# Kernel tuning notes

Measured on AMD Instinct MI355X. Metric: run time of the kernel, lower is better.

Reference implementation:

```python
import jax, jax.numpy as jnp
import numpy as np

N_HEAD = 16


def setup_inputs() -> dict:
    key = jax.random.key(0)
    ks = jax.random.split(key, 11)
    B, T, D = 8, 448, 1024
    init = 0.02
    x = jax.random.normal(ks[0], (B, T, D), dtype=jnp.float32)
    k_cache = jax.random.normal(ks[1], (B, T, D), dtype=jnp.float32)
    v_cache = jax.random.normal(ks[2], (B, T, D), dtype=jnp.float32)
    # Whisper-style additive causal mask: 0 on/below diagonal, large negative above
    mask = jnp.triu(jnp.full((T, T), -1e9, dtype=jnp.float32), k=1)
    Wq = jax.random.normal(ks[3], (D, D), dtype=jnp.float32) * init
    bq = jax.random.normal(ks[4], (D,), dtype=jnp.float32) * init
    Wk = jax.random.normal(ks[5], (D, D), dtype=jnp.float32) * init  # key proj has no bias
    Wv = jax.random.normal(ks[6], (D, D), dtype=jnp.float32) * init
    bv = jax.random.normal(ks[7], (D,), dtype=jnp.float32) * init
    Wo = jax.random.normal(ks[8], (D, D), dtype=jnp.float32) * init
    bo = jax.random.normal(ks[9], (D,), dtype=jnp.float32) * init
    return {"x": x, "k_cache": k_cache, "v_cache": v_cache, "mask": mask,
            "Wq": Wq, "bq": bq, "Wk": Wk, "Wv": Wv, "bv": bv, "Wo": Wo, "bo": bo}


def reference(x, k_cache, v_cache, mask, Wq, bq, Wk, Wv, bv, Wo, bo):
    # QKV projections (key has no bias, as in Whisper)
    q = x @ Wq + bq
    k = x @ Wk
    v = x @ Wv + bv
    # In-place KV cache append: write new keys/values into the tail of the cache
    T_new = k.shape[1]
    k_cache = k_cache.at[:, -T_new:, :].set(k)
    v_cache = v_cache.at[:, -T_new:, :].set(v)

    B, T, D = q.shape
    H = N_HEAD
    dh = D // H
    scale = dh ** (-0.25)  # applied to BOTH q and k

    qh = (q * scale).reshape(B, T, H, dh).transpose(0, 2, 1, 3)           # [B,H,T,dh]
    kh = (k_cache * scale).reshape(B, k_cache.shape[1], H, dh).transpose(0, 2, 1, 3)
    vh = v_cache.reshape(B, v_cache.shape[1], H, dh).transpose(0, 2, 1, 3)

    qk = jnp.einsum('bhqd,bhkd->bhqk', qh, kh) + mask[:T, :T]             # [B,H,T,Tc]
    qk = qk.astype(jnp.float32)  # upcast for softmax, matching original
    w = jax.nn.softmax(qk, axis=-1).astype(q.dtype)

    out = jnp.einsum('bhqk,bhkd->bhqd', w, vh)                            # [B,H,T,dh]
    out = out.transpose(0, 2, 1, 3).reshape(B, T, D)
    return out @ Wo + bo, k_cache, v_cache
```

## Files before the change

### kernel.cpp

```cpp
#include <hip/hip_runtime.h>
#include <hip/hip_bf16.h>
#include <math.h>

#define B 8
#define T 448
#define D 1024
#define H 16
#define DH 64
#define M (B*T)

typedef short short8 __attribute__((ext_vector_type(8)));
typedef float floatx4 __attribute__((ext_vector_type(4)));
typedef unsigned short u16;

__device__ __forceinline__ u16 f2bf(float f) {
    union { float f; unsigned u; } v; v.f = f;
    unsigned r = v.u + 0x7FFF + ((v.u >> 16) & 1);
    return (u16)(r >> 16);
}

__global__ __launch_bounds__(256) void xconv(const float* __restrict__ x, u16* __restrict__ xb) {
    const int i = blockIdx.x * 256 + threadIdx.x;
    float4 v = ((const float4*)x)[i];
    ushort4 o;
    o.x = f2bf(v.x); o.y = f2bf(v.y); o.z = f2bf(v.z); o.w = f2bf(v.w);
    ((ushort4*)xb)[i] = o;
}

__global__ __launch_bounds__(256) void wconv(const float* __restrict__ W, u16* __restrict__ Wt) {
    __shared__ float tile[64][65];
    const int k0 = blockIdx.y * 64, n0 = blockIdx.x * 64;
    const int tr = threadIdx.x >> 4;
    const int tc = threadIdx.x & 15;
    #pragma unroll
    for (int i = 0; i < 4; ++i) {
        float4 v = *(const float4*)(W + (size_t)(k0 + tr + 16 * i) * D + n0 + tc * 4);
        tile[tr + 16 * i][tc * 4 + 0] = v.x;
        tile[tr + 16 * i][tc * 4 + 1] = v.y;
        tile[tr + 16 * i][tc * 4 + 2] = v.z;
        tile[tr + 16 * i][tc * 4 + 3] = v.w;
    }
    __syncthreads();
    #pragma unroll
    for (int i = 0; i < 4; ++i) {
        const int n = tr + 16 * i;
        ushort4 o;
        o.x = f2bf(tile[tc * 4 + 0][n]);
        o.y = f2bf(tile[tc * 4 + 1][n]);
        o.z = f2bf(tile[tc * 4 + 2][n]);
        o.w = f2bf(tile[tc * 4 + 3][n]);
        *(ushort4*)(Wt + (size_t)(n0 + n) * D + k0 + tc * 4) = o;
    }
}

#define GBM 128
#define GBN 64
#define GBK 32
__global__ __launch_bounds__(256) void gemm_bt(
    const u16* __restrict__ A, const u16* __restrict__ Bt,
    const float* __restrict__ bias,
    float* __restrict__ Cf,
    u16* __restrict__ Cb)
{
    __shared__ u16 As[GBM][GBK + 8];
    __shared__ u16 Bs[GBN][GBK + 8];
    const int m0 = blockIdx.y * GBM;
    const int n0 = blockIdx.x * GBN;
    const int tid = threadIdx.x;
    const int wave = tid >> 6, lane = tid & 63;
    const int wy = wave >> 1, wx = wave & 1;
    const int lrow = lane & 15, lquad = lane >> 4;

    floatx4 acc[4][2];
    #pragma unroll
    for (int i = 0; i < 4; ++i)
        #pragma unroll
        for (int j = 0; j < 2; ++j)
            acc[i][j] = (floatx4){0.f, 0.f, 0.f, 0.f};

    const int sa = tid * 2;
    for (int k0 = 0; k0 < 1024; k0 += GBK) {
        short8 a0 = *(const short8*)(A + (size_t)(m0 + (sa >> 2)) * 1024 + k0 + (sa & 3) * 8);
        short8 a1 = *(const short8*)(A + (size_t)(m0 + ((sa + 1) >> 2)) * 1024 + k0 + ((sa + 1) & 3) * 8);
        short8 b0 = *(const short8*)(Bt + (size_t)(n0 + (tid >> 2)) * 1024 + k0 + (tid & 3) * 8);
        __syncthreads();
        *(short8*)&As[sa >> 2][(sa & 3) * 8] = a0;
        *(short8*)&As[(sa + 1) >> 2][((sa + 1) & 3) * 8] = a1;
        *(short8*)&Bs[tid >> 2][(tid & 3) * 8] = b0;
        __syncthreads();
        short8 af[4], bfr[2];
        #pragma unroll
        for (int i = 0; i < 4; ++i)
            af[i] = *(const short8*)&As[wy * 64 + i * 16 + lrow][lquad * 8];
        #pragma unroll
        for (int j = 0; j < 2; ++j)
            bfr[j] = *(const short8*)&Bs[wx * 32 + j * 16 + lrow][lquad * 8];
        #pragma unroll
        for (int i = 0; i < 4; ++i)
            #pragma unroll
            for (int j = 0; j < 2; ++j)
                acc[i][j] = __builtin_amdgcn_mfma_f32_16x16x32_bf16(af[i], bfr[j], acc[i][j], 0, 0, 0);
    }

    #pragma unroll
    for (int j = 0; j < 2; ++j) {
        const int col = n0 + wx * 32 + j * 16 + lrow;
        const float bb = bias ? bias[col] : 0.f;
        #pragma unroll
        for (int i = 0; i < 4; ++i) {
            #pragma unroll
            for (int r = 0; r < 4; ++r) {
                const int row = m0 + wy * 64 + i * 16 + lquad * 4 + r;
                const float v = acc[i][j][r] + bb;
                if (Cf) Cf[(size_t)row * 1024 + col] = v;
                if (Cb) Cb[(size_t)row * 1024 + col] = f2bf(v);
            }
        }
    }
}

__global__ __launch_bounds__(256) void flash_attn(
    const u16* __restrict__ Qb, const u16* __restrict__ Kb,
    const u16* __restrict__ Vb, u16* __restrict__ Ob)
{
    __shared__ u16 Qs[64][72];
    __shared__ u16 Ks[64][72];
    __shared__ u16 Vt[64][72];
    __shared__ u16 Pt[4][16][72];
    const int qt = blockIdx.x;
    const int bh = blockIdx.y;
    const int h = bh & (H - 1), b = bh >> 4;
    const int tid = threadIdx.x, wave = tid >> 6, lane = tid & 63;
    const int lrow = lane & 15, lquad = lane >> 4;
    const int q0 = qt * 64;

    const size_t hoff = (size_t)h * DH;
    const u16* qbase = Qb + (size_t)b * T * D + hoff;
    const u16* kbase = Kb + (size_t)b * T * D + hoff;
    const u16* vbase = Vb + (size_t)b * T * D + hoff;

    {
        const int s = tid * 2;
        short8 v0 = *(const short8*)(qbase + (size_t)(q0 + (s >> 3)) * D + (s & 7) * 8);
        short8 v1 = *(const short8*)(qbase + (size_t)(q0 + ((s + 1) >> 3)) * D + ((s + 1) & 7) * 8);
        *(short8*)&Qs[s >> 3][(s & 7) * 8] = v0;
        *(short8*)&Qs[(s + 1) >> 3][((s + 1) & 7) * 8] = v1;
    }
    __syncthreads();
    short8 aq0 = *(const short8*)&Qs[wave * 16 + lrow][lquad * 8];
    short8 aq1 = *(const short8*)&Qs[wave * 16 + lrow][32 + lquad * 8];

    float m_i[4], l_i[4];
    floatx4 oacc[4];
    #pragma unroll
    for (int r = 0; r < 4; ++r) { m_i[r] = -INFINITY; l_i[r] = 0.f; }
    #pragma unroll
    for (int n = 0; n < 4; ++n) oacc[n] = (floatx4){0.f, 0.f, 0.f, 0.f};

    const float SC = 0.125f * 1.44269504088896340736f;
    const int nkt = qt + 1;

    for (int kt = 0; kt < nkt; ++kt) {
        const int k0 = kt * 64;
        {
            const int s = tid * 2;
            const int r0 = s >> 3, o0 = (s & 7) * 8;
            const int r1 = (s + 1) >> 3, o1 = ((s + 1) & 7) * 8;
            short8 kv0 = *(const short8*)(kbase + (size_t)(k0 + r0) * D + o0);
            short8 kv1 = *(const short8*)(kbase + (size_t)(k0 + r1) * D + o1);
            short8 vv0 = *(const short8*)(vbase + (size_t)(k0 + r0) * D + o0);
            short8 vv1 = *(const short8*)(vbase + (size_t)(k0 + r1) * D + o1);
            __syncthreads();
            *(short8*)&Ks[r0][o0] = kv0;
            *(short8*)&Ks[r1][o1] = kv1;
            #pragma unroll
            for (int j = 0; j < 8; ++j) Vt[o0 + j][r0] = (u16)vv0[j];
            #pragma unroll
            for (int j = 0; j < 8; ++j) Vt[o1 + j][r1] = (u16)vv1[j];
        }
        __syncthreads();

        floatx4 s4[4];
        #pragma unroll
        for (int sub = 0; sub < 4; ++sub) {
            short8 bk0 = *(const short8*)&Ks[sub * 16 + lrow][lquad * 8];
            short8 bk1 = *(const short8*)&Ks[sub * 16 + lrow][32 + lquad * 8];
            floatx4 z = (floatx4){0.f, 0.f, 0.f, 0.f};
            z = __builtin_amdgcn_mfma_f32_16x16x32_bf16(aq0, bk0, z, 0, 0, 0);
            z = __builtin_amdgcn_mfma_f32_16x16x32_bf16(aq1, bk1, z, 0, 0, 0);
            s4[sub] = z;
        }

        float p[4][4];
        #pragma unroll
        for (int r = 0; r < 4; ++r) {
            const int qg = q0 + wave * 16 + lquad * 4 + r;
            float sv[4];
            float mx = -INFINITY;
            #pragma unroll
            for (int sub = 0; sub < 4; ++sub) {
                const int kk = k0 + sub * 16 + lrow;
                float v = s4[sub][r] * SC;
                v = (kk <= qg) ? v : -INFINITY;
                sv[sub] = v;
                mx = fmaxf(mx, v);
            }
            mx = fmaxf(mx, __shfl_xor(mx, 1));
            mx = fmaxf(mx, __shfl_xor(mx, 2));
            mx = fmaxf(mx, __shfl_xor(mx, 4));
            mx = fmaxf(mx, __shfl_xor(mx, 8));
            const float mnew = fmaxf(m_i[r], mx);
            const float alpha = exp2f(m_i[r] - mnew);
            float ls = 0.f;
            #pragma unroll
            for (int sub = 0; sub < 4; ++sub) {
                const float pv = exp2f(sv[sub] - mnew);
                p[sub][r] = pv;
                ls += pv;
            }
            ls += __shfl_xor(ls, 1);
            ls += __shfl_xor(ls, 2);
            ls += __shfl_xor(ls, 4);
            ls += __shfl_xor(ls, 8);
            l_i[r] = l_i[r] * alpha + ls;
            m_i[r] = mnew;
            #pragma unroll
            for (int n = 0; n < 4; ++n) oacc[n][r] *= alpha;
        }

        #pragma unroll
        for (int sub = 0; sub < 4; ++sub)
            #pragma unroll
            for (int r = 0; r < 4; ++r)
                Pt[wave][lquad * 4 + r][sub * 16 + lrow] = f2bf(p[sub][r]);
        __syncthreads();
        short8 ap0 = *(const short8*)&Pt[wave][lrow][lquad * 8];
        short8 ap1 = *(const short8*)&Pt[wave][lrow][32 + lquad * 8];

        #pragma unroll
        for (int n = 0; n < 4; ++n) {
            short8 bv0 = *(const short8*)&Vt[n * 16 + lrow][lquad * 8];
            short8 bv1 = *(const short8*)&Vt[n * 16 + lrow][32 + lquad * 8];
            oacc[n] = __builtin_amdgcn_mfma_f32_16x16x32_bf16(ap0, bv0, oacc[n], 0, 0, 0);
            oacc[n] = __builtin_amdgcn_mfma_f32_16x16x32_bf16(ap1, bv1, oacc[n], 0, 0, 0);
        }
    }

    #pragma unroll
    for (int r = 0; r < 4; ++r) {
        const float inv = 1.f / l_i[r];
        const int qg = q0 + wave * 16 + lquad * 4 + r;
        u16* orow = Ob + ((size_t)b * T + qg) * D + hoff;
        #pragma unroll
        for (int n = 0; n < 4; ++n)
            orow[n * 16 + lrow] = f2bf(oacc[n][r] * inv);
    }
}

extern "C" void kernel_launch(void* const* d_in, const int* in_sizes, int n_in,
                              void* d_out, int out_size, void* d_ws, size_t ws_size,
                              hipStream_t stream) {
    const float* x  = (const float*)d_in[0];
    const float* Wq = (const float*)d_in[4];
    const float* bq = (const float*)d_in[5];
    const float* Wk = (const float*)d_in[6];
    const float* Wv = (const float*)d_in[7];
    const float* bv = (const float*)d_in[8];
    const float* Wo = (const float*)d_in[9];
    const float* bo = (const float*)d_in[10];

    float* out  = (float*)d_out;
    float* kout = out + (size_t)M * D;
    float* vout = out + 2 * (size_t)M * D;

    u16* xb  = (u16*)d_ws;
    u16* qb  = xb  + (size_t)M * D;
    u16* kb  = qb  + (size_t)M * D;
    u16* vb  = kb  + (size_t)M * D;
    u16* ab  = vb  + (size_t)M * D;
    u16* wtq = ab  + (size_t)M * D;
    u16* wtk = wtq + (size_t)D * D;
    u16* wtv = wtk + (size_t)D * D;
    u16* wto = wtv + (size_t)D * D;

    xconv<<<M * D / 1024, 256, 0, stream>>>(x, xb);
    dim3 wg(16, 16);
    wconv<<<wg, 256, 0, stream>>>(Wq, wtq);
    wconv<<<wg, 256, 0, stream>>>(Wk, wtk);
    wconv<<<wg, 256, 0, stream>>>(Wv, wtv);
    wconv<<<wg, 256, 0, stream>>>(Wo, wto);

    dim3 gg(D / GBN, M / GBM);
    gemm_bt<<<gg, 256, 0, stream>>>(xb, wtq, bq,      nullptr, qb);
    gemm_bt<<<gg, 256, 0, stream>>>(xb, wtk, nullptr, kout,    kb);
    gemm_bt<<<gg, 256, 0, stream>>>(xb, wtv, bv,      vout,    vb);

    flash_attn<<<dim3(7, 128), 256, 0, stream>>>(qb, kb, vb, ab);

    gemm_bt<<<gg, 256, 0, stream>>>(ab, wto, bo, out, nullptr);
}
```

Measured before the change: 235.5 us.

## Fuse QKV GEMMs, batch weight conversion, use LDS-direct loads and pre-transposed V

The four weight-conversion launches are merged into one 3D-grid kernel, and the three QKV projections become a single GEMM over a concatenated 3072-wide weight. The GEMM tile grows to 128x128 and tiles are loaded with global_load_lds straight into unpadded shared memory. The V projection epilogue writes a transposed bf16 copy, so the attention kernel loads V tiles with vector stores instead of scalar transposes. The aim is fewer launches, more reuse per tile and cheaper V staging, at the cost of unpadded LDS (possible bank conflicts), strided scattered vbT stores and higher register pressure.

```diff
diff --git a/kernel.cpp b/kernel.cpp
--- a/kernel.cpp
+++ b/kernel.cpp
@@ -19,6 +19,12 @@
     return (u16)(r >> 16);
 }
 
+__device__ __forceinline__ void gload16(const void* gptr, void* lptr) {
+    __builtin_amdgcn_global_load_lds(
+        (const __attribute__((address_space(1))) void*)gptr,
+        (__attribute__((address_space(3))) void*)lptr, 16, 0, 0);
+}
+
 __global__ __launch_bounds__(256) void xconv(const float* __restrict__ x, u16* __restrict__ xb) {
     const int i = blockIdx.x * 256 + threadIdx.x;
     float4 v = ((const float4*)x)[i];
@@ -27,11 +33,17 @@
     ((ushort4*)xb)[i] = o;
 }
 
-__global__ __launch_bounds__(256) void wconv(const float* __restrict__ W, u16* __restrict__ Wt) {
+__global__ __launch_bounds__(256) void wconv4(
+    const float* __restrict__ Wq, const float* __restrict__ Wk,
+    const float* __restrict__ Wv, const float* __restrict__ Wo,
+    u16* __restrict__ wt)
+{
     __shared__ float tile[64][65];
+    const int z = blockIdx.z;
+    const float* W = (z == 0) ? Wq : (z == 1) ? Wk : (z == 2) ? Wv : Wo;
+    u16* Wt = wt + (size_t)z * D * D;
     const int k0 = blockIdx.y * 64, n0 = blockIdx.x * 64;
-    const int tr = threadIdx.x >> 4;
-    const int tc = threadIdx.x & 15;
+    const int tr = threadIdx.x >> 4, tc = threadIdx.x & 15;
     #pragma unroll
     for (int i = 0; i < 4; ++i) {
         float4 v = *(const float4*)(W + (size_t)(k0 + tr + 16 * i) * D + n0 + tc * 4);
@@ -53,75 +65,93 @@
     }
 }
 
-#define GBM 128
-#define GBN 64
-#define GBK 32
-__global__ __launch_bounds__(256) void gemm_bt(
-    const u16* __restrict__ A, const u16* __restrict__ Bt,
-    const float* __restrict__ bias,
-    float* __restrict__ Cf,
-    u16* __restrict__ Cb)
+__global__ __launch_bounds__(256) void gemm128(
+    const u16* __restrict__ A, const u16* __restrict__ Bt, int mode,
+    const float* __restrict__ bq, const float* __restrict__ bv,
+    u16* __restrict__ qkvb, float* __restrict__ kout, float* __restrict__ vout,
+    u16* __restrict__ vbT,
+    const float* __restrict__ bo, float* __restrict__ outp)
 {
-    __shared__ u16 As[GBM][GBK + 8];
-    __shared__ u16 Bs[GBN][GBK + 8];
-    const int m0 = blockIdx.y * GBM;
-    const int n0 = blockIdx.x * GBN;
+    __shared__ u16 As[128][32];
+    __shared__ u16 Bs[128][32];
+    const int m0 = blockIdx.y * 128;
+    const int n0 = blockIdx.x * 128;
     const int tid = threadIdx.x;
     const int wave = tid >> 6, lane = tid & 63;
     const int wy = wave >> 1, wx = wave & 1;
     const int lrow = lane & 15, lquad = lane >> 4;
 
-    floatx4 acc[4][2];
+    floatx4 acc[4][4];
     #pragma unroll
     for (int i = 0; i < 4; ++i)
         #pragma unroll
-        for (int j = 0; j < 2; ++j)
+        for (int j = 0; j < 4; ++j)
             acc[i][j] = (floatx4){0.f, 0.f, 0.f, 0.f};
 
-    const int sa = tid * 2;
-    for (int k0 = 0; k0 < 1024; k0 += GBK) {
-        short8 a0 = *(const short8*)(A + (size_t)(m0 + (sa >> 2)) * 1024 + k0 + (sa & 3) * 8);
-        short8 a1 = *(const short8*)(A + (size_t)(m0 + ((sa + 1) >> 2)) * 1024 + k0 + ((sa + 1) & 3) * 8);
-        short8 b0 = *(const short8*)(Bt + (size_t)(n0 + (tid >> 2)) * 1024 + k0 + (tid & 3) * 8);
+    const u16* agp0 = A + (size_t)(m0 + (tid >> 2)) * 1024 + (tid & 3) * 8;
+    const u16* agp1 = agp0 + (size_t)64 * 1024;
+    const u16* bgp0 = Bt + (size_t)(n0 + (tid >> 2)) * 1024 + (tid & 3) * 8;
+    const u16* bgp1 = bgp0 + (size_t)64 * 1024;
+    char* lA0 = (char*)&As[0][0] + wave * 1024;
+    char* lA1 = lA0 + 4096;
+    char* lB0 = (char*)&Bs[0][0] + wave * 1024;
+    char* lB1 = lB0 + 4096;
+
+    for (int k0 = 0; k0 < 1024; k0 += 32) {
         __syncthreads();
-        *(short8*)&As[sa >> 2][(sa & 3) * 8] = a0;
-        *(short8*)&As[(sa + 1) >> 2][((sa + 1) & 3) * 8] = a1;
-        *(short8*)&Bs[tid >> 2][(tid & 3) * 8] = b0;
+        gload16(agp0 + k0, lA0);
+        gload16(agp1 + k0, lA1);
+        gload16(bgp0 + k0, lB0);
+        gload16(bgp1 + k0, lB1);
         __syncthreads();
-        short8 af[4], bfr[2];
+        short8 af[4], bfr[4];
         #pragma unroll
         for (int i = 0; i < 4; ++i)
             af[i] = *(const short8*)&As[wy * 64 + i * 16 + lrow][lquad * 8];
         #pragma unroll
-        for (int j = 0; j < 2; ++j)
-            bfr[j] = *(const short8*)&Bs[wx * 32 + j * 16 + lrow][lquad * 8];
+        for (int j = 0; j < 4; ++j)
+            bfr[j] = *(const short8*)&Bs[wx * 64 + j * 16 + lrow][lquad * 8];
         #pragma unroll
         for (int i = 0; i < 4; ++i)
             #pragma unroll
-            for (int j = 0; j < 2; ++j)
+            for (int j = 0; j < 4; ++j)
                 acc[i][j] = __builtin_amdgcn_mfma_f32_16x16x32_bf16(af[i], bfr[j], acc[i][j], 0, 0, 0);
     }
 
-    #pragma unroll
-    for (int j = 0; j < 2; ++j) {
-        const int col = n0 + wx * 32 + j * 16 + lrow;
-        const float bb = bias ? bias[col] : 0.f;
+    const int sec = (mode == 0) ? (n0 >> 10) : 3;
+    #pragma unroll
+    for (int j = 0; j < 4; ++j) {
+        const int col = n0 + wx * 64 + j * 16 + lrow;
+        float bb;
+        if (mode == 1) bb = bo[col];
+        else bb = (sec == 0) ? bq[col] : (sec == 2 ? bv[col - 2048] : 0.f);
         #pragma unroll
         for (int i = 0; i < 4; ++i) {
             #pragma unroll
             for (int r = 0; r < 4; ++r) {
                 const int row = m0 + wy * 64 + i * 16 + lquad * 4 + r;
                 const float v = acc[i][j][r] + bb;
-                if (Cf) Cf[(size_t)row * 1024 + col] = v;
-                if (Cb) Cb[(size_t)row * 1024 + col] = f2bf(v);
+                if (mode == 1) {
+                    outp[(size_t)row * 1024 + col] = v;
+                } else if (sec == 0) {
+                    qkvb[(size_t)row * 3072 + col] = f2bf(v);
+                } else if (sec == 1) {
+                    qkvb[(size_t)row * 3072 + col] = f2bf(v);
+                    kout[(size_t)row * 1024 + col - 1024] = v;
+                } else {
+                    vout[(size_t)row * 1024 + col - 2048] = v;
+                    const int bidx = row / 448, tt = row - bidx * 448;
+                    vbT[((size_t)bidx * 1024 + (col - 2048)) * 448 + tt] = f2bf(v);
+                }
             }
         }
     }
 }
 
 __global__ __launch_bounds__(256) void flash_attn(
-    const u16* __restrict__ Qb, const u16* __restrict__ Kb,
-    const u16* __restrict__ Vb, u16* __restrict__ Ob)
+    const u16* __restrict__ QKVb,
+    const u16* __restrict__ VbT,
+    u16* __restrict__ Ob)
 {
     __shared__ u16 Qs[64][72];
     __shared__ u16 Ks[64][72];
@@ -134,15 +164,14 @@
     const int lrow = lane & 15, lquad = lane >> 4;
     const int q0 = qt * 64;
 
-    const size_t hoff = (size_t)h * DH;
-    const u16* qbase = Qb + (size_t)b * T * D + hoff;
-    const u16* kbase = Kb + (size_t)b * T * D + hoff;
-    const u16* vbase = Vb + (size_t)b * T * D + hoff;
+    const u16* qbase = QKVb + (size_t)b * T * 3072 + (size_t)h * DH;
+    const u16* kbase = qbase + 1024;
+    const u16* vtb   = VbT + (size_t)bh * DH * T;
 
     {
         const int s = tid * 2;
-        short8 v0 = *(const short8*)(qbase + (size_t)(q0 + (s >> 3)) * D + (s & 7) * 8);
-        short8 v1 = *(const short8*)(qbase + (size_t)(q0 + ((s + 1) >> 3)) * D + ((s + 1) & 7) * 8);
+        short8 v0 = *(const short8*)(qbase + (size_t)(q0 + (s >> 3)) * 3072 + (s & 7) * 8);
+        short8 v1 = *(const short8*)(qbase + (size_t)(q0 + ((s + 1) >> 3)) * 3072 + ((s + 1) & 7) * 8);
         *(short8*)&Qs[s >> 3][(s & 7) * 8] = v0;
         *(short8*)&Qs[(s + 1) >> 3][((s + 1) & 7) * 8] = v1;
     }
@@ -166,17 +195,15 @@
             const int s = tid * 2;
             const int r0 = s >> 3, o0 = (s & 7) * 8;
             const int r1 = (s + 1) >> 3, o1 = ((s + 1) & 7) * 8;
-            short8 kv0 = *(const short8*)(kbase + (size_t)(k0 + r0) * D + o0);
-            short8 kv1 = *(const short8*)(kbase + (size_t)(k0 + r1) * D + o1);
-            short8 vv0 = *(const short8*)(vbase + (size_t)(k0 + r0) * D + o0);
-            short8 vv1 = *(const short8*)(vbase + (size_t)(k0 + r1) * D + o1);
+            short8 kv0 = *(const short8*)(kbase + (size_t)(k0 + r0) * 3072 + o0);
+            short8 kv1 = *(const short8*)(kbase + (size_t)(k0 + r1) * 3072 + o1);
+            short8 vv0 = *(const short8*)(vtb + (size_t)r0 * T + k0 + o0);
+            short8 vv1 = *(const short8*)(vtb + (size_t)r1 * T + k0 + o1);
             __syncthreads();
             *(short8*)&Ks[r0][o0] = kv0;
             *(short8*)&Ks[r1][o1] = kv1;
-            #pragma unroll
-            for (int j = 0; j < 8; ++j) Vt[o0 + j][r0] = (u16)vv0[j];
-            #pragma unroll
-            for (int j = 0; j < 8; ++j) Vt[o1 + j][r1] = (u16)vv1[j];
+            *(short8*)&Vt[r0][o0] = vv0;
+            *(short8*)&Vt[r1][o1] = vv1;
         }
         __syncthreads();
 
@@ -250,7 +277,7 @@
     for (int r = 0; r < 4; ++r) {
         const float inv = 1.f / l_i[r];
         const int qg = q0 + wave * 16 + lquad * 4 + r;
-        u16* orow = Ob + ((size_t)b * T + qg) * D + hoff;
+        u16* orow = Ob + ((size_t)b * T + qg) * D + (size_t)h * DH;
         #pragma unroll
         for (int n = 0; n < 4; ++n)
             orow[n * 16 + lrow] = f2bf(oacc[n][r] * inv);
@@ -273,29 +300,20 @@
     float* kout = out + (size_t)M * D;
     float* vout = out + 2 * (size_t)M * D;
 
-    u16* xb  = (u16*)d_ws;
-    u16* qb  = xb  + (size_t)M * D;
-    u16* kb  = qb  + (size_t)M * D;
-    u16* vb  = kb  + (size_t)M * D;
-    u16* ab  = vb  + (size_t)M * D;
-    u16* wtq = ab  + (size_t)M * D;
-    u16* wtk = wtq + (size_t)D * D;
-    u16* wtv = wtk + (size_t)D * D;
-    u16* wto = wtv + (size_t)D * D;
+    u16* xb   = (u16*)d_ws;
+    u16* wt   = xb   + (size_t)M * D;
+    u16* qkvb = wt   + (size_t)4 * D * D;
+    u16* vbT  = qkvb + (size_t)M * 3 * D;
+    u16* ab   = vbT  + (size_t)M * D;
 
     xconv<<<M * D / 1024, 256, 0, stream>>>(x, xb);
-    dim3 wg(16, 16);
-    wconv<<<wg, 256, 0, stream>>>(Wq, wtq);
-    wconv<<<wg, 256, 0, stream>>>(Wk, wtk);
-    wconv<<<wg, 256, 0, stream>>>(Wv, wtv);
-    wconv<<<wg, 256, 0, stream>>>(Wo, wto);
-
-    dim3 gg(D / GBN, M / GBM);
-    gemm_bt<<<gg, 256, 0, stream>>>(xb, wtq, bq,      nullptr, qb);
-    gemm_bt<<<gg, 256, 0, stream>>>(xb, wtk, nullptr, kout,    kb);
-    gemm_bt<<<gg, 256, 0, stream>>>(xb, wtv, bv,      vout,    vb);
-
-    flash_attn<<<dim3(7, 128), 256, 0, stream>>>(qb, kb, vb, ab);
-
-    gemm_bt<<<gg, 256, 0, stream>>>(ab, wto, bo, out, nullptr);
-}
+    wconv4<<<dim3(16, 16, 4), 256, 0, stream>>>(Wq, Wk, Wv, Wo, wt);
+
+    gemm128<<<dim3(24, 28), 256, 0, stream>>>(xb, wt, 0, bq, bv,
+                                              qkvb, kout, vout, vbT, nullptr, nullptr);
+
+    flash_attn<<<dim3(7, 128), 256, 0, stream>>>(qkvb, vbT, ab);
+
+    gemm128<<<dim3(8, 28), 256, 0, stream>>>(ab, wt + (size_t)3 * D * D, 1, nullptr, nullptr,
+                                             nullptr, nullptr, nullptr, nullptr, bo, out);
+}
```

Measured after the change: 210.3 us. 10.7% less time.
